# Kernel optimization log

Measured on AMD Instinct MI355X. Metric: run time of the kernel, lower is better.

Reference implementation:

```python
import jax, jax.numpy as jnp
import numpy as np

B, T, C = 4, 2048, 512
H, CDR_HEADS = 8, 2
D = C // H


def setup_inputs() -> dict:
    key = jax.random.key(0)
    ks = jax.random.split(key, 12)
    s = 1.0 / np.sqrt(C)
    return {
        "x": jax.random.normal(ks[0], (B, T, C), dtype=jnp.float32),
        "mask": jax.random.randint(ks[1], (B, T), 0, 2, dtype=jnp.int32),
        "cdrs_score": jax.random.randint(ks[2], (B, T), 0, 2, dtype=jnp.int32),
        "Wq": jax.random.normal(ks[3], (C, C), dtype=jnp.float32) * s,
        "bq": jnp.zeros((C,), dtype=jnp.float32),
        "Wk": jax.random.normal(ks[4], (C, C), dtype=jnp.float32) * s,
        "bk": jnp.zeros((C,), dtype=jnp.float32),
        "Wv": jax.random.normal(ks[5], (C, C), dtype=jnp.float32) * s,
        "bv": jnp.zeros((C,), dtype=jnp.float32),
        "Wo": jax.random.normal(ks[6], (C, C), dtype=jnp.float32) * s,
        "bo": jnp.zeros((C,), dtype=jnp.float32),
    }


def reference(x, mask, cdrs_score, Wq, bq, Wk, bk, Wv, bv, Wo, bo):
    # projections -> [B, H, T, D]
    def heads(y):
        return y.reshape(B, T, H, D).transpose(0, 2, 1, 3)

    q = heads(x @ Wq + bq)
    k = heads(x @ Wk + bk)
    v = heads(x @ Wv + bv)

    scores = jnp.einsum("bhqd,bhkd->bhqk", q, k) / jnp.sqrt(jnp.float32(D))

    # padding mask: keys with mask==0 are invalid for all heads
    pad = (mask == 0)[:, None, None, :]                      # [B,1,1,T]
    scores = jnp.where(pad, -jnp.inf, scores)

    # CDR key mask for the first CDR_HEADS heads; disabled if a sample has no CDR tokens
    cdr_key_mask = (cdrs_score == 0)                          # [B, T]
    all_masked = jnp.all(cdr_key_mask, axis=-1, keepdims=True)  # [B, 1]
    cdr_key_mask = jnp.where(all_masked, False, cdr_key_mask)   # [B, T]
    head_is_cdr = (jnp.arange(H) < CDR_HEADS)[None, :, None, None]  # [1,H,1,1]
    cdr_full = head_is_cdr & cdr_key_mask[:, None, None, :]         # [B,H,1,T]
    scores = jnp.where(cdr_full, -jnp.inf, scores)

    attn = jax.nn.softmax(scores, axis=-1)                    # [B,H,T,T]
    ctx = jnp.einsum("bhqk,bhkd->bhqd", attn, v)
    ctx = ctx.transpose(0, 2, 1, 3).reshape(B, T, C)
    return ctx @ Wo + bo
```

## Files before the change

### kernel.cpp

```cpp
#include <hip/hip_runtime.h>
#include <math.h>

#define B_ 4
#define T_ 2048
#define C_ 512
#define H_ 8
#define D_ 64
#define CDR_HEADS_ 2
#define NROWS (B_ * T_)

typedef unsigned short ush;
typedef __bf16  bf16x8 __attribute__((ext_vector_type(8)));
typedef float   f32x4  __attribute__((ext_vector_type(4)));

#define MFMA16(a, b, c) __builtin_amdgcn_mfma_f32_16x16x32_bf16((a), (b), (c), 0, 0, 0)

static __device__ __forceinline__ ush f2bf(float f) {
    unsigned u = __float_as_uint(f);
    u += 0x7FFF + ((u >> 16) & 1);
    return (ush)(u >> 16);
}
static __device__ __forceinline__ float bf2f(ush h) {
    return __uint_as_float(((unsigned)h) << 16);
}

static __device__ __forceinline__ void gload16(const void* gsrc, void* ldst) {
    __builtin_amdgcn_global_load_lds(
        (const __attribute__((address_space(1))) unsigned int*)gsrc,
        (__attribute__((address_space(3))) unsigned int*)ldst, 16, 0, 0);
}

__global__ __launch_bounds__(256) void compact_kernel(
    const int* __restrict__ mask, const int* __restrict__ cdrs,
    int* __restrict__ klist, int* __restrict__ kcnt) {
    __shared__ int s_any;
    __shared__ int sa[256], sb[256];
    const int b = blockIdx.x, tid = threadIdx.x;
    if (tid == 0) s_any = 0;
    __syncthreads();

    int m8[8], c8[8];
    int any = 0, ca = 0;
    const int base = b * T_ + tid * 8;
#pragma unroll
    for (int i = 0; i < 8; ++i) {
        m8[i] = mask[base + i];
        c8[i] = cdrs[base + i];
        any |= c8[i];
        ca += (m8[i] != 0);
    }
    if (any) s_any = 1;
    __syncthreads();
    const int en = s_any;

    int cb = 0;
#pragma unroll
    for (int i = 0; i < 8; ++i)
        cb += (m8[i] != 0 && (!en || c8[i] != 0));

    sa[tid] = ca; sb[tid] = cb;
    __syncthreads();
    for (int off = 1; off < 256; off <<= 1) {
        int va = 0, vb = 0;
        if (tid >= off) { va = sa[tid - off]; vb = sb[tid - off]; }
        __syncthreads();
        sa[tid] += va; sb[tid] += vb;
        __syncthreads();
    }

    int offA = sa[tid] - ca;
    int offB = sb[tid] - cb;
    int* la = klist + (size_t)(b * 2 + 0) * T_;
    int* lb = klist + (size_t)(b * 2 + 1) * T_;
#pragma unroll
    for (int i = 0; i < 8; ++i) {
        const int t = tid * 8 + i;
        if (m8[i] != 0) la[offA++] = t;
        if (m8[i] != 0 && (!en || c8[i] != 0)) lb[offB++] = t;
    }
    if (tid == 255) {
        kcnt[b * 2 + 0] = sa[255];
        kcnt[b * 2 + 1] = sb[255];
    }
}

__global__ __launch_bounds__(256) void decomp_a_kernel(
    const float* __restrict__ src, ush* __restrict__ Dh, ush* __restrict__ Dl) {
    const int id = blockIdx.x * 256 + threadIdx.x;
    const int m = id >> 6, kc = id & 63;
    const float* p = src + (size_t)m * C_ + kc * 8;
    const float4 a = ((const float4*)p)[0];
    const float4 b2 = ((const float4*)p)[1];
    float xv[8] = {a.x, a.y, a.z, a.w, b2.x, b2.y, b2.z, b2.w};
    union { ush u[8]; int4 q; } hi, lo;
#pragma unroll
    for (int i = 0; i < 8; ++i) {
        const ush h = f2bf(xv[i]);
        hi.u[i] = h;
        lo.u[i] = f2bf(xv[i] - bf2f(h));
    }
    const int mt = m >> 7, ml = m & 127, kt = kc >> 2, cidx = kc & 3;
    const size_t tbase = ((size_t)mt * 16 + kt) * 4096;
    const int boff = ml * 64 + ((cidx ^ ((ml >> 1) & 3)) << 4);
    *(int4*)((char*)(Dh + tbase) + boff) = hi.q;
    *(int4*)((char*)(Dl + tbase) + boff) = lo.q;
}

__global__ __launch_bounds__(256) void decomp_w_kernel(
    const float* __restrict__ W0, const float* __restrict__ W1,
    const float* __restrict__ W2, const float* __restrict__ W3,
    ush* __restrict__ Wth, ush* __restrict__ Wtl) {
    const int mat = blockIdx.y;
    const float* W = (mat == 0) ? W0 : (mat == 1) ? W1 : (mat == 2) ? W2 : W3;
    const int id = blockIdx.x * 256 + threadIdx.x;
    const int n = id & 511, kc = id >> 9;
    float xv[8];
#pragma unroll
    for (int j = 0; j < 8; ++j)
        xv[j] = W[(size_t)(kc * 8 + j) * C_ + n];
    union { ush u[8]; int4 q; } hi, lo;
#pragma unroll
    for (int i = 0; i < 8; ++i) {
        const ush h = f2bf(xv[i]);
        hi.u[i] = h;
        lo.u[i] = f2bf(xv[i] - bf2f(h));
    }
    const int nt = n >> 7, nl = n & 127, kt = kc >> 2, cidx = kc & 3;
    const size_t tbase = (size_t)mat * 262144 + ((size_t)nt * 16 + kt) * 4096;
    const int boff = nl * 64 + ((cidx ^ ((nl >> 1) & 3)) << 4);
    *(int4*)((char*)(Wth + tbase) + boff) = hi.q;
    *(int4*)((char*)(Wtl + tbase) + boff) = lo.q;
}

template <int OUTMODE>
static __device__ __forceinline__ void gemm3_body(
    const ush* __restrict__ Ah_g, const ush* __restrict__ Al_g,
    const ush* __restrict__ Bh_g, const ush* __restrict__ Bl_g,
    const float* __restrict__ bias, void* __restrict__ outp, float scale) {
    __shared__ char lds[32768];
    char* const sAh = lds;
    char* const sAl = lds + 8192;
    char* const sBh = lds + 16384;
    char* const sBl = lds + 24576;

    const int tid = threadIdx.x;
    const int lane = tid & 63, w = tid >> 6;
    const int g = lane >> 4, l15 = lane & 15;
    const int wr = w >> 1, wc = w & 1;
    const int mt = blockIdx.x, nt = blockIdx.y;

    const char* gAh = (const char*)Ah_g + (size_t)(mt * 16) * 8192;
    const char* gAl = (const char*)Al_g + (size_t)(mt * 16) * 8192;
    const char* gBh = (const char*)Bh_g + (size_t)(nt * 16) * 8192;
    const char* gBl = (const char*)Bl_g + (size_t)(nt * 16) * 8192;

    f32x4 acc[4][4];
#pragma unroll
    for (int i = 0; i < 4; ++i)
#pragma unroll
        for (int j = 0; j < 4; ++j)
#pragma unroll
            for (int r = 0; r < 4; ++r) acc[i][j][r] = 0.f;

    const int lw = w * 2048;
    for (int kt = 0; kt < 16; ++kt) {
        __syncthreads();
        const size_t gb = (size_t)kt * 8192 + lw + lane * 16;
        gload16(gAh + gb,        sAh + lw);
        gload16(gAh + gb + 1024, sAh + lw + 1024);
        gload16(gAl + gb,        sAl + lw);
        gload16(gAl + gb + 1024, sAl + lw + 1024);
        gload16(gBh + gb,        sBh + lw);
        gload16(gBh + gb + 1024, sBh + lw + 1024);
        gload16(gBl + gb,        sBl + lw);
        gload16(gBl + gb + 1024, sBl + lw + 1024);
        __syncthreads();

        bf16x8 fah[4], fal[4], fbh[4], fbl[4];
#pragma unroll
        for (int rb = 0; rb < 4; ++rb) {
            const int row = wr * 64 + rb * 16 + l15;
            const int off = row * 64 + ((g ^ ((row >> 1) & 3)) << 4);
            fah[rb] = __builtin_bit_cast(bf16x8, *(const int4*)(sAh + off));
            fal[rb] = __builtin_bit_cast(bf16x8, *(const int4*)(sAl + off));
        }
#pragma unroll
        for (int cb = 0; cb < 4; ++cb) {
            const int row = wc * 64 + cb * 16 + l15;
            const int off = row * 64 + ((g ^ ((row >> 1) & 3)) << 4);
            fbh[cb] = __builtin_bit_cast(bf16x8, *(const int4*)(sBh + off));
            fbl[cb] = __builtin_bit_cast(bf16x8, *(const int4*)(sBl + off));
        }
#pragma unroll
        for (int rb = 0; rb < 4; ++rb)
#pragma unroll
            for (int cb = 0; cb < 4; ++cb) {
                acc[rb][cb] = MFMA16(fah[rb], fbh[cb], acc[rb][cb]);
                acc[rb][cb] = MFMA16(fah[rb], fbl[cb], acc[rb][cb]);
                acc[rb][cb] = MFMA16(fal[rb], fbh[cb], acc[rb][cb]);
            }
    }

    const int mbase = mt * 128 + wr * 64;
    const int nbase = nt * 128 + wc * 64;
    float bcol[4];
#pragma unroll
    for (int cb = 0; cb < 4; ++cb) bcol[cb] = bias[nbase + cb * 16 + l15];

#pragma unroll
    for (int rb = 0; rb < 4; ++rb)
#pragma unroll
        for (int cb = 0; cb < 4; ++cb) {
            const int colg = nbase + cb * 16 + l15;
#pragma unroll
            for (int r = 0; r < 4; ++r) {
                const int m = mbase + rb * 16 + g * 4 + r;
                const float vv = acc[rb][cb][r] + bcol[cb];
                if (OUTMODE == 0) {
                    ((float*)outp)[(size_t)m * C_ + colg] = vv;
                } else {
                    const int bb = m >> 11, t = m & (T_ - 1);
                    const int h = colg >> 6, d = colg & 63;
                    ((ush*)outp)[(((size_t)(bb * H_ + h) * T_ + t) * D_) + d] =
                        f2bf(vv * scale);
                }
            }
        }
}

__global__ __launch_bounds__(256) void gemm3_qkv_kernel(
    const ush* __restrict__ Xh, const ush* __restrict__ Xl,
    const ush* __restrict__ Wth, const ush* __restrict__ Wtl,
    const float* __restrict__ bq, const float* __restrict__ bk,
    const float* __restrict__ bv,
    ush* __restrict__ Qb, ush* __restrict__ Kb, ush* __restrict__ Vb) {
    const int z = blockIdx.z;
    const ush* bh = Wth + (size_t)z * 262144;
    const ush* bl = Wtl + (size_t)z * 262144;
    if (z == 0)      gemm3_body<1>(Xh, Xl, bh, bl, bq, Qb, 0.125f);
    else if (z == 1) gemm3_body<1>(Xh, Xl, bh, bl, bk, Kb, 1.0f);
    else             gemm3_body<1>(Xh, Xl, bh, bl, bv, Vb, 1.0f);
}

__global__ __launch_bounds__(256) void gemm3_out_kernel(
    const ush* __restrict__ Ch, const ush* __restrict__ Cl,
    const ush* __restrict__ Wth, const ush* __restrict__ Wtl,
    const float* __restrict__ bo, float* __restrict__ out) {
    gemm3_body<0>(Ch, Cl, Wth + (size_t)3 * 262144, Wtl + (size_t)3 * 262144,
                  bo, out, 1.0f);
}

__global__ __launch_bounds__(256) void gather_kernel(
    const ush* __restrict__ Kb, const ush* __restrict__ Vb,
    const int* __restrict__ klist, const int* __restrict__ kcnt,
    ush* __restrict__ Kc, ush* __restrict__ Vct) {
    __shared__ ush Vs[64 * 72];
    const int tid = threadIdx.x;
    const int ti = blockIdx.x, h = blockIdx.y, b = blockIdx.z;
    const int sel = (h < CDR_HEADS_) ? 1 : 0;
    const int NV = kcnt[b * 2 + sel];
    if (ti * 64 >= NV) return;
    const int* __restrict__ list = klist + (size_t)(b * 2 + sel) * T_;
    const size_t bh = (size_t)b * H_ + h;
    const ush* kb_ = Kb + bh * T_ * D_;
    const ush* vb_ = Vb + bh * T_ * D_;
    ush* kt = Kc + bh * (32 * 4096) + (size_t)ti * 4096;
    ush* vt = Vct + bh * (32 * 4096) + (size_t)ti * 4096;

    const int i = tid >> 2, c = tid & 3;
    const int pos = ti * 64 + i;
    int4 kv0 = {0,0,0,0}, kv1 = {0,0,0,0}, vv0 = {0,0,0,0}, vv1 = {0,0,0,0};
    if (pos < NV) {
        const int row = list[pos];
        const int4* kr = (const int4*)(kb_ + (size_t)row * D_ + c * 16);
        kv0 = kr[0]; kv1 = kr[1];
        const int4* vr = (const int4*)(vb_ + (size_t)row * D_ + c * 16);
        vv0 = vr[0]; vv1 = vr[1];
    }
    {
        const int s0 = (c * 2) ^ (i & 7), s1 = (c * 2 + 1) ^ (i & 7);
        *(int4*)(kt + i * 64 + s0 * 8) = kv0;
        *(int4*)(kt + i * 64 + s1 * 8) = kv1;
    }
    *(int4*)(Vs + i * 72 + c * 16)     = vv0;
    *(int4*)(Vs + i * 72 + c * 16 + 8) = vv1;
    __syncthreads();
    {
        const int d = tid >> 2, c2 = tid & 3;
        union { ush u[16]; int4 q[2]; } pk;
#pragma unroll
        for (int ii = 0; ii < 16; ++ii)
            pk.u[ii] = Vs[(c2 * 16 + ii) * 72 + d];
        const int s0 = (c2 * 2) ^ (d & 7), s1 = (c2 * 2 + 1) ^ (d & 7);
        *(int4*)(vt + d * 64 + s0 * 8) = pk.q[0];
        *(int4*)(vt + d * 64 + s1 * 8) = pk.q[1];
    }
}

__global__ __launch_bounds__(256) void attn_mfma_kernel(
    const ush* __restrict__ Qb, const ush* __restrict__ Kc,
    const ush* __restrict__ Vct, const int* __restrict__ kcnt,
    float* __restrict__ ctx) {
    __shared__ ush Ks[2][4096];
    __shared__ ush Vts[2][4096];
    __shared__ ush Pl[4 * 32 * 72];

    const int tid = threadIdx.x;
    const int lane = tid & 63, w = tid >> 6;
    const int g = lane >> 4, l15 = lane & 15;
    const int qt = blockIdx.x, h = blockIdx.y, b = blockIdx.z;
    const int sel = (h < CDR_HEADS_) ? 1 : 0;
    const int NV = kcnt[b * 2 + sel];
    const int ntiles = (NV + 63) >> 6;
    const size_t bh = (size_t)b * H_ + h;
    const int swz = (l15 & 7) << 4;

    bf16x8 aq[2][2];
    {
        const ush* qp = Qb + (bh * T_ + (size_t)qt * 128 + w * 32) * D_;
#pragma unroll
        for (int qb = 0; qb < 2; ++qb)
#pragma unroll
            for (int kc = 0; kc < 2; ++kc) {
                int4 t4 = *(const int4*)(qp + (qb * 16 + l15) * D_ + kc * 32 + g * 8);
                aq[qb][kc] = __builtin_bit_cast(bf16x8, t4);
            }
    }

    f32x4 cacc[2][4];
#pragma unroll
    for (int qb = 0; qb < 2; ++qb)
#pragma unroll
        for (int db = 0; db < 4; ++db)
#pragma unroll
            for (int r = 0; r < 4; ++r) cacc[qb][db][r] = 0.f;
    float mr[2] = {-INFINITY, -INFINITY};
    float lr[2] = {0.f, 0.f};

    const char* ktiles = (const char*)(Kc + bh * (32 * 4096));
    const char* vtiles = (const char*)(Vct + bh * (32 * 4096));
    ush* Pw = Pl + w * (32 * 72);
    const int lw = w * 1024;

    gload16(ktiles + lw * 2 + lane * 16, &Ks[0][lw]);
    gload16(ktiles + lw * 2 + 1024 + lane * 16, &Ks[0][lw + 512]);
    gload16(vtiles + lw * 2 + lane * 16, &Vts[0][lw]);
    gload16(vtiles + lw * 2 + 1024 + lane * 16, &Vts[0][lw + 512]);
    __syncthreads();

    for (int t = 0; t < ntiles; ++t) {
        const int cur = t & 1, nxt = cur ^ 1;
        if (t + 1 < ntiles) {
            const char* gk = ktiles + (size_t)(t + 1) * 8192 + lw * 2 + lane * 16;
            const char* gv = vtiles + (size_t)(t + 1) * 8192 + lw * 2 + lane * 16;
            gload16(gk, &Ks[nxt][lw]);
            gload16(gk + 1024, &Ks[nxt][lw + 512]);
            gload16(gv, &Vts[nxt][lw]);
            gload16(gv + 1024, &Vts[nxt][lw + 512]);
        }

        bf16x8 bk[4][2];
#pragma unroll
        for (int j = 0; j < 4; ++j) {
            const int rowb = (j * 16 + l15) * 128;
            bk[j][0] = __builtin_bit_cast(bf16x8,
                *(const int4*)((const char*)Ks[cur] + ((rowb + g * 16) ^ swz)));
            bk[j][1] = __builtin_bit_cast(bf16x8,
                *(const int4*)((const char*)Ks[cur] + ((rowb + 64 + g * 16) ^ swz)));
        }
        f32x4 s[2][4];
        const f32x4 z4 = {0.f, 0.f, 0.f, 0.f};
        __builtin_amdgcn_s_setprio(1);
#pragma unroll
        for (int j = 0; j < 4; ++j) s[0][j] = MFMA16(bk[j][0], aq[0][0], z4);
#pragma unroll
        for (int j = 0; j < 4; ++j) s[1][j] = MFMA16(bk[j][0], aq[1][0], z4);
#pragma unroll
        for (int j = 0; j < 4; ++j) s[0][j] = MFMA16(bk[j][1], aq[0][1], s[0][j]);
#pragma unroll
        for (int j = 0; j < 4; ++j) s[1][j] = MFMA16(bk[j][1], aq[1][1], s[1][j]);
        __builtin_amdgcn_s_setprio(0);

        const int kb0 = t * 64;
        if (kb0 + 64 > NV) {
#pragma unroll
            for (int j = 0; j < 4; ++j)
#pragma unroll
                for (int r = 0; r < 4; ++r)
                    if (kb0 + j * 16 + g * 4 + r >= NV) {
                        s[0][j][r] = -INFINITY;
                        s[1][j][r] = -INFINITY;
                    }
        }

        float rq[2];
#pragma unroll
        for (int qb = 0; qb < 2; ++qb) {
            float mx = s[qb][0][0];
#pragma unroll
            for (int j = 0; j < 4; ++j)
#pragma unroll
                for (int r = 0; r < 4; ++r) mx = fmaxf(mx, s[qb][j][r]);
            mx = fmaxf(mx, __shfl_xor(mx, 16));
            mx = fmaxf(mx, __shfl_xor(mx, 32));
            const float mn = fmaxf(mr[qb], mx);
            rq[qb] = __expf(mr[qb] - mn);
            mr[qb] = mn;
            float sum = 0.f;
#pragma unroll
            for (int j = 0; j < 4; ++j)
#pragma unroll
                for (int r = 0; r < 4; ++r) {
                    const float p = __expf(s[qb][j][r] - mn);
                    s[qb][j][r] = p;
                    sum += p;
                }
            sum += __shfl_xor(sum, 16);
            sum += __shfl_xor(sum, 32);
            lr[qb] = lr[qb] * rq[qb] + sum;
        }

#pragma unroll
        for (int qb = 0; qb < 2; ++qb)
#pragma unroll
            for (int r = 0; r < 4; ++r) {
                const float rr = __shfl(rq[qb], g * 4 + r, 16);
#pragma unroll
                for (int db = 0; db < 4; ++db) cacc[qb][db][r] *= rr;
            }

#pragma unroll
        for (int qb = 0; qb < 2; ++qb) {
            unsigned* prow = (unsigned*)(Pw + (qb * 16 + l15) * 72);
#pragma unroll
            for (int j = 0; j < 4; ++j) {
                const unsigned p01 = (unsigned)f2bf(s[qb][j][0]) |
                                     ((unsigned)f2bf(s[qb][j][1]) << 16);
                const unsigned p23 = (unsigned)f2bf(s[qb][j][2]) |
                                     ((unsigned)f2bf(s[qb][j][3]) << 16);
                prow[(j * 16 + g * 4) >> 1] = p01;
                prow[(j * 16 + g * 4 + 2) >> 1] = p23;
            }
        }

        __builtin_amdgcn_s_setprio(1);
#pragma unroll
        for (int kc = 0; kc < 2; ++kc) {
            bf16x8 pa0 = __builtin_bit_cast(bf16x8,
                *(const int4*)(Pw + l15 * 72 + kc * 32 + g * 8));
            bf16x8 pa1 = __builtin_bit_cast(bf16x8,
                *(const int4*)(Pw + (16 + l15) * 72 + kc * 32 + g * 8));
#pragma unroll
            for (int db = 0; db < 4; ++db) {
                bf16x8 vbf = __builtin_bit_cast(bf16x8,
                    *(const int4*)((const char*)Vts[cur] +
                        ((((db * 16 + l15) * 128) + kc * 64 + g * 16) ^ swz)));
                cacc[0][db] = MFMA16(pa0, vbf, cacc[0][db]);
                cacc[1][db] = MFMA16(pa1, vbf, cacc[1][db]);
            }
        }
        __builtin_amdgcn_s_setprio(0);

        __syncthreads();
    }

    const size_t trow = (size_t)b * T_ + (size_t)qt * 128 + w * 32;
#pragma unroll
    for (int qb = 0; qb < 2; ++qb)
#pragma unroll
        for (int r = 0; r < 4; ++r) {
            const float lrq = __shfl(lr[qb], g * 4 + r, 16);
            const float inv = 1.f / lrq;
            float* orow = ctx + (trow + qb * 16 + g * 4 + r) * C_ + h * D_;
#pragma unroll
            for (int db = 0; db < 4; ++db)
                orow[db * 16 + l15] = cacc[qb][db][r] * inv;
        }
}

extern "C" void kernel_launch(void* const* d_in, const int* in_sizes, int n_in,
                              void* d_out, int out_size, void* d_ws, size_t ws_size,
                              hipStream_t stream) {
    const float* x    = (const float*)d_in[0];
    const int*   mask = (const int*)d_in[1];
    const int*   cdrs = (const int*)d_in[2];
    const float* Wq   = (const float*)d_in[3];
    const float* bq   = (const float*)d_in[4];
    const float* Wk   = (const float*)d_in[5];
    const float* bk   = (const float*)d_in[6];
    const float* Wv   = (const float*)d_in[7];
    const float* bv   = (const float*)d_in[8];
    const float* Wo   = (const float*)d_in[9];
    const float* bo   = (const float*)d_in[10];
    float* out = (float*)d_out;

    const size_t per = (size_t)B_ * H_ * T_ * D_;
    ush* Qb  = (ush*)d_ws;
    ush* Kb  = Qb + per;
    ush* Vb  = Kb + per;
    ush* Kc  = Vb + per;
    ush* Vct = Kc + per;
    ush* Xh  = Vct + per;
    ush* Xl  = Xh + per;
    ush* Wth = Xl + per;
    ush* Wtl = Wth + 4 * 262144;
    int* klist = (int*)(Wtl + 4 * 262144);
    int* kcnt  = klist + (size_t)B_ * 2 * T_;
    float* ctxf = (float*)Kb;

    compact_kernel<<<B_, 256, 0, stream>>>(mask, cdrs, klist, kcnt);

    decomp_a_kernel<<<2048, 256, 0, stream>>>(x, Xh, Xl);
    decomp_w_kernel<<<dim3(128, 4), 256, 0, stream>>>(Wq, Wk, Wv, Wo, Wth, Wtl);

    gemm3_qkv_kernel<<<dim3(64, 4, 3), 256, 0, stream>>>(
        Xh, Xl, Wth, Wtl, bq, bk, bv, Qb, Kb, Vb);

    gather_kernel<<<dim3(32, H_, B_), 256, 0, stream>>>(Kb, Vb, klist, kcnt,
                                                        Kc, Vct);

    attn_mfma_kernel<<<dim3(T_ / 128, H_, B_), 256, 0, stream>>>(
        Qb, Kc, Vct, kcnt, ctxf);

    decomp_a_kernel<<<2048, 256, 0, stream>>>(ctxf, Xh, Xl);

    gemm3_out_kernel<<<dim3(64, 4), 256, 0, stream>>>(Xh, Xl, Wth, Wtl, bo, out);
}
```

Measured before the change: 222.9 us.

## Merge prep kernels and fuse ctx bf16 split into attention epilogue

Merges the mask compaction and the x and W bf16 hi/lo decomposition kernels into one prep launch. The attention kernel now writes ctx directly as swizzled bf16 hi/lo tiles, which removes the fp32 ctx round trip and the second decomposition kernel. Attention is also restructured to 512 threads with 16 query rows per wave. It remaps blocks in a flat 1D grid, adds a lazy rescale that skips the online-softmax correction when the running max rises by at most 8, and uses an XOR-swizzled P buffer. The cost is scattered 2-byte global stores in the epilogue and more waves per block sharing the same LDS K/V tiles.

```diff
diff --git a/kernel.cpp b/kernel.cpp
--- a/kernel.cpp
+++ b/kernel.cpp
@@ -30,106 +30,104 @@
         (__attribute__((address_space(3))) unsigned int*)ldst, 16, 0, 0);
 }
 
-__global__ __launch_bounds__(256) void compact_kernel(
+__global__ __launch_bounds__(256) void prep_kernel(
+    const float* __restrict__ x,
+    const float* __restrict__ W0, const float* __restrict__ W1,
+    const float* __restrict__ W2, const float* __restrict__ W3,
     const int* __restrict__ mask, const int* __restrict__ cdrs,
+    ush* __restrict__ Xh, ush* __restrict__ Xl,
+    ush* __restrict__ Wth, ush* __restrict__ Wtl,
     int* __restrict__ klist, int* __restrict__ kcnt) {
     __shared__ int s_any;
     __shared__ int sa[256], sb[256];
-    const int b = blockIdx.x, tid = threadIdx.x;
-    if (tid == 0) s_any = 0;
-    __syncthreads();
-
-    int m8[8], c8[8];
-    int any = 0, ca = 0;
-    const int base = b * T_ + tid * 8;
-#pragma unroll
-    for (int i = 0; i < 8; ++i) {
-        m8[i] = mask[base + i];
-        c8[i] = cdrs[base + i];
-        any |= c8[i];
-        ca += (m8[i] != 0);
-    }
-    if (any) s_any = 1;
-    __syncthreads();
-    const int en = s_any;
-
-    int cb = 0;
-#pragma unroll
-    for (int i = 0; i < 8; ++i)
-        cb += (m8[i] != 0 && (!en || c8[i] != 0));
-
-    sa[tid] = ca; sb[tid] = cb;
-    __syncthreads();
-    for (int off = 1; off < 256; off <<= 1) {
-        int va = 0, vb = 0;
-        if (tid >= off) { va = sa[tid - off]; vb = sb[tid - off]; }
+    const int bid = blockIdx.x, tid = threadIdx.x;
+
+    if (bid < 2048) {
+        const int id = bid * 256 + tid;
+        const int m = id >> 6, kc = id & 63;
+        const float* p = x + (size_t)m * C_ + kc * 8;
+        const float4 a = ((const float4*)p)[0];
+        const float4 b2 = ((const float4*)p)[1];
+        float xv[8] = {a.x, a.y, a.z, a.w, b2.x, b2.y, b2.z, b2.w};
+        union { ush u[8]; int4 q; } hi, lo;
+#pragma unroll
+        for (int i = 0; i < 8; ++i) {
+            const ush h = f2bf(xv[i]);
+            hi.u[i] = h;
+            lo.u[i] = f2bf(xv[i] - bf2f(h));
+        }
+        const int mt = m >> 7, ml = m & 127, kt = kc >> 2, cidx = kc & 3;
+        const size_t tbase = ((size_t)mt * 16 + kt) * 4096;
+        const int boff = ml * 64 + ((cidx ^ ((ml >> 1) & 3)) << 4);
+        *(int4*)((char*)(Xh + tbase) + boff) = hi.q;
+        *(int4*)((char*)(Xl + tbase) + boff) = lo.q;
+    } else if (bid < 2560) {
+        const int z = bid - 2048;
+        const int mat = z >> 7;
+        const float* W = (mat == 0) ? W0 : (mat == 1) ? W1 : (mat == 2) ? W2 : W3;
+        const int id = (z & 127) * 256 + tid;
+        const int n = id & 511, kc = id >> 9;
+        float xv[8];
+#pragma unroll
+        for (int j = 0; j < 8; ++j)
+            xv[j] = W[(size_t)(kc * 8 + j) * C_ + n];
+        union { ush u[8]; int4 q; } hi, lo;
+#pragma unroll
+        for (int i = 0; i < 8; ++i) {
+            const ush h = f2bf(xv[i]);
+            hi.u[i] = h;
+            lo.u[i] = f2bf(xv[i] - bf2f(h));
+        }
+        const int nt = n >> 7, nl = n & 127, kt = kc >> 2, cidx = kc & 3;
+        const size_t tbase = (size_t)mat * 262144 + ((size_t)nt * 16 + kt) * 4096;
+        const int boff = nl * 64 + ((cidx ^ ((nl >> 1) & 3)) << 4);
+        *(int4*)((char*)(Wth + tbase) + boff) = hi.q;
+        *(int4*)((char*)(Wtl + tbase) + boff) = lo.q;
+    } else {
+        const int b = bid - 2560;
+        if (tid == 0) s_any = 0;
         __syncthreads();
-        sa[tid] += va; sb[tid] += vb;
+        int m8[8], c8[8];
+        int any = 0, ca = 0;
+        const int base = b * T_ + tid * 8;
+#pragma unroll
+        for (int i = 0; i < 8; ++i) {
+            m8[i] = mask[base + i];
+            c8[i] = cdrs[base + i];
+            any |= c8[i];
+            ca += (m8[i] != 0);
+        }
+        if (any) s_any = 1;
         __syncthreads();
-    }
-
-    int offA = sa[tid] - ca;
-    int offB = sb[tid] - cb;
-    int* la = klist + (size_t)(b * 2 + 0) * T_;
-    int* lb = klist + (size_t)(b * 2 + 1) * T_;
-#pragma unroll
-    for (int i = 0; i < 8; ++i) {
-        const int t = tid * 8 + i;
-        if (m8[i] != 0) la[offA++] = t;
-        if (m8[i] != 0 && (!en || c8[i] != 0)) lb[offB++] = t;
-    }
-    if (tid == 255) {
-        kcnt[b * 2 + 0] = sa[255];
-        kcnt[b * 2 + 1] = sb[255];
-    }
-}
-
-__global__ __launch_bounds__(256) void decomp_a_kernel(
-    const float* __restrict__ src, ush* __restrict__ Dh, ush* __restrict__ Dl) {
-    const int id = blockIdx.x * 256 + threadIdx.x;
-    const int m = id >> 6, kc = id & 63;
-    const float* p = src + (size_t)m * C_ + kc * 8;
-    const float4 a = ((const float4*)p)[0];
-    const float4 b2 = ((const float4*)p)[1];
-    float xv[8] = {a.x, a.y, a.z, a.w, b2.x, b2.y, b2.z, b2.w};
-    union { ush u[8]; int4 q; } hi, lo;
-#pragma unroll
-    for (int i = 0; i < 8; ++i) {
-        const ush h = f2bf(xv[i]);
-        hi.u[i] = h;
-        lo.u[i] = f2bf(xv[i] - bf2f(h));
-    }
-    const int mt = m >> 7, ml = m & 127, kt = kc >> 2, cidx = kc & 3;
-    const size_t tbase = ((size_t)mt * 16 + kt) * 4096;
-    const int boff = ml * 64 + ((cidx ^ ((ml >> 1) & 3)) << 4);
-    *(int4*)((char*)(Dh + tbase) + boff) = hi.q;
-    *(int4*)((char*)(Dl + tbase) + boff) = lo.q;
-}
-
-__global__ __launch_bounds__(256) void decomp_w_kernel(
-    const float* __restrict__ W0, const float* __restrict__ W1,
-    const float* __restrict__ W2, const float* __restrict__ W3,
-    ush* __restrict__ Wth, ush* __restrict__ Wtl) {
-    const int mat = blockIdx.y;
-    const float* W = (mat == 0) ? W0 : (mat == 1) ? W1 : (mat == 2) ? W2 : W3;
-    const int id = blockIdx.x * 256 + threadIdx.x;
-    const int n = id & 511, kc = id >> 9;
-    float xv[8];
-#pragma unroll
-    for (int j = 0; j < 8; ++j)
-        xv[j] = W[(size_t)(kc * 8 + j) * C_ + n];
-    union { ush u[8]; int4 q; } hi, lo;
-#pragma unroll
-    for (int i = 0; i < 8; ++i) {
-        const ush h = f2bf(xv[i]);
-        hi.u[i] = h;
-        lo.u[i] = f2bf(xv[i] - bf2f(h));
-    }
-    const int nt = n >> 7, nl = n & 127, kt = kc >> 2, cidx = kc & 3;
-    const size_t tbase = (size_t)mat * 262144 + ((size_t)nt * 16 + kt) * 4096;
-    const int boff = nl * 64 + ((cidx ^ ((nl >> 1) & 3)) << 4);
-    *(int4*)((char*)(Wth + tbase) + boff) = hi.q;
-    *(int4*)((char*)(Wtl + tbase) + boff) = lo.q;
+        const int en = s_any;
+        int cb = 0;
+#pragma unroll
+        for (int i = 0; i < 8; ++i)
+            cb += (m8[i] != 0 && (!en || c8[i] != 0));
+        sa[tid] = ca; sb[tid] = cb;
+        __syncthreads();
+        for (int off = 1; off < 256; off <<= 1) {
+            int va = 0, vb = 0;
+            if (tid >= off) { va = sa[tid - off]; vb = sb[tid - off]; }
+            __syncthreads();
+            sa[tid] += va; sb[tid] += vb;
+            __syncthreads();
+        }
+        int offA = sa[tid] - ca;
+        int offB = sb[tid] - cb;
+        int* la = klist + (size_t)(b * 2 + 0) * T_;
+        int* lb = klist + (size_t)(b * 2 + 1) * T_;
+#pragma unroll
+        for (int i = 0; i < 8; ++i) {
+            const int t = tid * 8 + i;
+            if (m8[i] != 0) la[offA++] = t;
+            if (m8[i] != 0 && (!en || c8[i] != 0)) lb[offB++] = t;
+        }
+        if (tid == 255) {
+            kcnt[b * 2 + 0] = sa[255];
+            kcnt[b * 2 + 1] = sb[255];
+        }
+    }
 }
 
 template <int OUTMODE>
@@ -297,66 +295,62 @@
     }
 }
 
-__global__ __launch_bounds__(256) void attn_mfma_kernel(
+__global__ __launch_bounds__(512) void attn_mfma_kernel(
     const ush* __restrict__ Qb, const ush* __restrict__ Kc,
     const ush* __restrict__ Vct, const int* __restrict__ kcnt,
-    float* __restrict__ ctx) {
+    ush* __restrict__ Xh, ush* __restrict__ Xl) {
     __shared__ ush Ks[2][4096];
     __shared__ ush Vts[2][4096];
-    __shared__ ush Pl[4 * 32 * 72];
+    __shared__ ush Pl[8192];
 
     const int tid = threadIdx.x;
     const int lane = tid & 63, w = tid >> 6;
     const int g = lane >> 4, l15 = lane & 15;
-    const int qt = blockIdx.x, h = blockIdx.y, b = blockIdx.z;
+
+    const int i = blockIdx.x;
+    const int x7 = i & 7, local = i >> 3;
+    const int b = local >> 4;
+    const int h = (x7 - 2 * b) & 7;
+    const int qt = local & 15;
+    const int bh = b * H_ + h;
+
     const int sel = (h < CDR_HEADS_) ? 1 : 0;
     const int NV = kcnt[b * 2 + sel];
     const int ntiles = (NV + 63) >> 6;
-    const size_t bh = (size_t)b * H_ + h;
     const int swz = (l15 & 7) << 4;
 
-    bf16x8 aq[2][2];
+    bf16x8 aq[2];
     {
-        const ush* qp = Qb + (bh * T_ + (size_t)qt * 128 + w * 32) * D_;
-#pragma unroll
-        for (int qb = 0; qb < 2; ++qb)
-#pragma unroll
-            for (int kc = 0; kc < 2; ++kc) {
-                int4 t4 = *(const int4*)(qp + (qb * 16 + l15) * D_ + kc * 32 + g * 8);
-                aq[qb][kc] = __builtin_bit_cast(bf16x8, t4);
-            }
-    }
-
-    f32x4 cacc[2][4];
-#pragma unroll
-    for (int qb = 0; qb < 2; ++qb)
-#pragma unroll
-        for (int db = 0; db < 4; ++db)
-#pragma unroll
-            for (int r = 0; r < 4; ++r) cacc[qb][db][r] = 0.f;
-    float mr[2] = {-INFINITY, -INFINITY};
-    float lr[2] = {0.f, 0.f};
-
-    const char* ktiles = (const char*)(Kc + bh * (32 * 4096));
-    const char* vtiles = (const char*)(Vct + bh * (32 * 4096));
-    ush* Pw = Pl + w * (32 * 72);
-    const int lw = w * 1024;
-
-    gload16(ktiles + lw * 2 + lane * 16, &Ks[0][lw]);
-    gload16(ktiles + lw * 2 + 1024 + lane * 16, &Ks[0][lw + 512]);
-    gload16(vtiles + lw * 2 + lane * 16, &Vts[0][lw]);
-    gload16(vtiles + lw * 2 + 1024 + lane * 16, &Vts[0][lw + 512]);
+        const ush* qp = Qb + ((size_t)bh * T_ + qt * 128 + w * 16) * D_;
+#pragma unroll
+        for (int kc = 0; kc < 2; ++kc)
+            aq[kc] = __builtin_bit_cast(bf16x8,
+                *(const int4*)(qp + l15 * D_ + kc * 32 + g * 8));
+    }
+
+    f32x4 cacc[4];
+#pragma unroll
+    for (int db = 0; db < 4; ++db)
+#pragma unroll
+        for (int r = 0; r < 4; ++r) cacc[db][r] = 0.f;
+    float mr = -INFINITY, lr = 0.f;
+
+    const char* ktiles = (const char*)(Kc + (size_t)bh * (32 * 4096));
+    const char* vtiles = (const char*)(Vct + (size_t)bh * (32 * 4096));
+    char* Pw = (char*)Pl + w * 2048;
+    const int lwo = w * 512;
+
+    gload16(ktiles + lwo * 2 + lane * 16, &Ks[0][lwo]);
+    gload16(vtiles + lwo * 2 + lane * 16, &Vts[0][lwo]);
     __syncthreads();
 
     for (int t = 0; t < ntiles; ++t) {
         const int cur = t & 1, nxt = cur ^ 1;
         if (t + 1 < ntiles) {
-            const char* gk = ktiles + (size_t)(t + 1) * 8192 + lw * 2 + lane * 16;
-            const char* gv = vtiles + (size_t)(t + 1) * 8192 + lw * 2 + lane * 16;
-            gload16(gk, &Ks[nxt][lw]);
-            gload16(gk + 1024, &Ks[nxt][lw + 512]);
-            gload16(gv, &Vts[nxt][lw]);
-            gload16(gv + 1024, &Vts[nxt][lw + 512]);
+            gload16(ktiles + (size_t)(t + 1) * 8192 + lwo * 2 + lane * 16,
+                    &Ks[nxt][lwo]);
+            gload16(vtiles + (size_t)(t + 1) * 8192 + lwo * 2 + lane * 16,
+                    &Vts[nxt][lwo]);
         }
 
         bf16x8 bk[4][2];
@@ -368,17 +362,13 @@
             bk[j][1] = __builtin_bit_cast(bf16x8,
                 *(const int4*)((const char*)Ks[cur] + ((rowb + 64 + g * 16) ^ swz)));
         }
-        f32x4 s[2][4];
+        f32x4 s[4];
         const f32x4 z4 = {0.f, 0.f, 0.f, 0.f};
         __builtin_amdgcn_s_setprio(1);
 #pragma unroll
-        for (int j = 0; j < 4; ++j) s[0][j] = MFMA16(bk[j][0], aq[0][0], z4);
-#pragma unroll
-        for (int j = 0; j < 4; ++j) s[1][j] = MFMA16(bk[j][0], aq[1][0], z4);
-#pragma unroll
-        for (int j = 0; j < 4; ++j) s[0][j] = MFMA16(bk[j][1], aq[0][1], s[0][j]);
-#pragma unroll
-        for (int j = 0; j < 4; ++j) s[1][j] = MFMA16(bk[j][1], aq[1][1], s[1][j]);
+        for (int j = 0; j < 4; ++j) s[j] = MFMA16(bk[j][0], aq[0], z4);
+#pragma unroll
+        for (int j = 0; j < 4; ++j) s[j] = MFMA16(bk[j][1], aq[1], s[j]);
         __builtin_amdgcn_s_setprio(0);
 
         const int kb0 = t * 64;
@@ -387,95 +377,94 @@
             for (int j = 0; j < 4; ++j)
 #pragma unroll
                 for (int r = 0; r < 4; ++r)
-                    if (kb0 + j * 16 + g * 4 + r >= NV) {
-                        s[0][j][r] = -INFINITY;
-                        s[1][j][r] = -INFINITY;
-                    }
-        }
-
-        float rq[2];
-#pragma unroll
-        for (int qb = 0; qb < 2; ++qb) {
-            float mx = s[qb][0][0];
-#pragma unroll
-            for (int j = 0; j < 4; ++j)
-#pragma unroll
-                for (int r = 0; r < 4; ++r) mx = fmaxf(mx, s[qb][j][r]);
-            mx = fmaxf(mx, __shfl_xor(mx, 16));
-            mx = fmaxf(mx, __shfl_xor(mx, 32));
-            const float mn = fmaxf(mr[qb], mx);
-            rq[qb] = __expf(mr[qb] - mn);
-            mr[qb] = mn;
-            float sum = 0.f;
-#pragma unroll
-            for (int j = 0; j < 4; ++j)
-#pragma unroll
-                for (int r = 0; r < 4; ++r) {
-                    const float p = __expf(s[qb][j][r] - mn);
-                    s[qb][j][r] = p;
-                    sum += p;
-                }
-            sum += __shfl_xor(sum, 16);
-            sum += __shfl_xor(sum, 32);
-            lr[qb] = lr[qb] * rq[qb] + sum;
-        }
-
-#pragma unroll
-        for (int qb = 0; qb < 2; ++qb)
+                    if (kb0 + j * 16 + g * 4 + r >= NV) s[j][r] = -INFINITY;
+        }
+
+        float pmax = s[0][0];
+#pragma unroll
+        for (int j = 0; j < 4; ++j)
+#pragma unroll
+            for (int r = 0; r < 4; ++r) pmax = fmaxf(pmax, s[j][r]);
+        pmax = fmaxf(pmax, __shfl_xor(pmax, 16));
+        pmax = fmaxf(pmax, __shfl_xor(pmax, 32));
+        if (!__all(pmax <= mr + 8.f)) {
+            const float mn = fmaxf(mr, pmax);
+            const float rr = __expf(mr - mn);
+            mr = mn;
+            lr *= rr;
 #pragma unroll
             for (int r = 0; r < 4; ++r) {
-                const float rr = __shfl(rq[qb], g * 4 + r, 16);
-#pragma unroll
-                for (int db = 0; db < 4; ++db) cacc[qb][db][r] *= rr;
+                const float rrq = __shfl(rr, g * 4 + r, 16);
+#pragma unroll
+                for (int db = 0; db < 4; ++db) cacc[db][r] *= rrq;
             }
-
-#pragma unroll
-        for (int qb = 0; qb < 2; ++qb) {
-            unsigned* prow = (unsigned*)(Pw + (qb * 16 + l15) * 72);
-#pragma unroll
-            for (int j = 0; j < 4; ++j) {
-                const unsigned p01 = (unsigned)f2bf(s[qb][j][0]) |
-                                     ((unsigned)f2bf(s[qb][j][1]) << 16);
-                const unsigned p23 = (unsigned)f2bf(s[qb][j][2]) |
-                                     ((unsigned)f2bf(s[qb][j][3]) << 16);
-                prow[(j * 16 + g * 4) >> 1] = p01;
-                prow[(j * 16 + g * 4 + 2) >> 1] = p23;
+        }
+        float sum = 0.f;
+#pragma unroll
+        for (int j = 0; j < 4; ++j)
+#pragma unroll
+            for (int r = 0; r < 4; ++r) {
+                const float p = __expf(s[j][r] - mr);
+                s[j][r] = p;
+                sum += p;
             }
-        }
-
+        sum += __shfl_xor(sum, 16);
+        sum += __shfl_xor(sum, 32);
+        lr += sum;
+
+#pragma unroll
+        for (int j = 0; j < 4; ++j) {
+            const ush u0 = __builtin_bit_cast(ush, (__bf16)s[j][0]);
+            const ush u1 = __builtin_bit_cast(ush, (__bf16)s[j][1]);
+            const ush u2 = __builtin_bit_cast(ush, (__bf16)s[j][2]);
+            const ush u3 = __builtin_bit_cast(ush, (__bf16)s[j][3]);
+            uint2 pk;
+            pk.x = (unsigned)u0 | ((unsigned)u1 << 16);
+            pk.y = (unsigned)u2 | ((unsigned)u3 << 16);
+            const int sb = (j * 2 + (g >> 1)) ^ (l15 & 7);
+            *(uint2*)(Pw + l15 * 128 + sb * 16 + (g & 1) * 8) = pk;
+        }
+
+        bf16x8 pa[2];
+#pragma unroll
+        for (int kc = 0; kc < 2; ++kc)
+            pa[kc] = __builtin_bit_cast(bf16x8,
+                *(const int4*)(Pw + l15 * 128 + (((kc * 4 + g) ^ (l15 & 7)) << 4)));
         __builtin_amdgcn_s_setprio(1);
 #pragma unroll
-        for (int kc = 0; kc < 2; ++kc) {
-            bf16x8 pa0 = __builtin_bit_cast(bf16x8,
-                *(const int4*)(Pw + l15 * 72 + kc * 32 + g * 8));
-            bf16x8 pa1 = __builtin_bit_cast(bf16x8,
-                *(const int4*)(Pw + (16 + l15) * 72 + kc * 32 + g * 8));
+        for (int kc = 0; kc < 2; ++kc)
 #pragma unroll
             for (int db = 0; db < 4; ++db) {
                 bf16x8 vbf = __builtin_bit_cast(bf16x8,
                     *(const int4*)((const char*)Vts[cur] +
                         ((((db * 16 + l15) * 128) + kc * 64 + g * 16) ^ swz)));
-                cacc[0][db] = MFMA16(pa0, vbf, cacc[0][db]);
-                cacc[1][db] = MFMA16(pa1, vbf, cacc[1][db]);
+                cacc[db] = MFMA16(pa[kc], vbf, cacc[db]);
             }
-        }
         __builtin_amdgcn_s_setprio(0);
 
         __syncthreads();
     }
 
-    const size_t trow = (size_t)b * T_ + (size_t)qt * 128 + w * 32;
-#pragma unroll
-    for (int qb = 0; qb < 2; ++qb)
-#pragma unroll
-        for (int r = 0; r < 4; ++r) {
-            const float lrq = __shfl(lr[qb], g * 4 + r, 16);
-            const float inv = 1.f / lrq;
-            float* orow = ctx + (trow + qb * 16 + g * 4 + r) * C_ + h * D_;
-#pragma unroll
-            for (int db = 0; db < 4; ++db)
-                orow[db * 16 + l15] = cacc[qb][db][r] * inv;
-        }
+    const int mt = b * 16 + qt;
+#pragma unroll
+    for (int r = 0; r < 4; ++r) {
+        const float lrq = __shfl(lr, g * 4 + r, 16);
+        const float inv = 1.f / lrq;
+        const int ml = w * 16 + g * 4 + r;
+#pragma unroll
+        for (int db = 0; db < 4; ++db) {
+            const int col = h * 64 + db * 16 + l15;
+            const float val = cacc[db][r] * inv;
+            const __bf16 hb = (__bf16)val;
+            const __bf16 lb2 = (__bf16)(val - (float)hb);
+            const int kt2 = col >> 5;
+            const int cidx = (col >> 3) & 3;
+            const size_t tb = ((size_t)mt * 16 + kt2) * 4096;
+            const int boff = ml * 64 + ((cidx ^ ((ml >> 1) & 3)) << 4) + (l15 & 7) * 2;
+            *(ush*)((char*)(Xh + tb) + boff) = __builtin_bit_cast(ush, hb);
+            *(ush*)((char*)(Xl + tb) + boff) = __builtin_bit_cast(ush, lb2);
+        }
+    }
 }
 
 extern "C" void kernel_launch(void* const* d_in, const int* in_sizes, int n_in,
@@ -506,12 +495,9 @@
     ush* Wtl = Wth + 4 * 262144;
     int* klist = (int*)(Wtl + 4 * 262144);
     int* kcnt  = klist + (size_t)B_ * 2 * T_;
-    float* ctxf = (float*)Kb;
-
-    compact_kernel<<<B_, 256, 0, stream>>>(mask, cdrs, klist, kcnt);
-
-    decomp_a_kernel<<<2048, 256, 0, stream>>>(x, Xh, Xl);
-    decomp_w_kernel<<<dim3(128, 4), 256, 0, stream>>>(Wq, Wk, Wv, Wo, Wth, Wtl);
+
+    prep_kernel<<<2564, 256, 0, stream>>>(x, Wq, Wk, Wv, Wo, mask, cdrs,
+                                          Xh, Xl, Wth, Wtl, klist, kcnt);
 
     gemm3_qkv_kernel<<<dim3(64, 4, 3), 256, 0, stream>>>(
         Xh, Xl, Wth, Wtl, bq, bk, bv, Qb, Kb, Vb);
@@ -519,10 +505,7 @@
     gather_kernel<<<dim3(32, H_, B_), 256, 0, stream>>>(Kb, Vb, klist, kcnt,
                                                         Kc, Vct);
 
-    attn_mfma_kernel<<<dim3(T_ / 128, H_, B_), 256, 0, stream>>>(
-        Qb, Kc, Vct, kcnt, ctxf);
-
-    decomp_a_kernel<<<2048, 256, 0, stream>>>(ctxf, Xh, Xl);
+    attn_mfma_kernel<<<512, 512, 0, stream>>>(Qb, Kc, Vct, kcnt, Xh, Xl);
 
     gemm3_out_kernel<<<dim3(64, 4), 256, 0, stream>>>(Xh, Xl, Wth, Wtl, bo, out);
 }
```

After: 198.5 us. -10.9%, faster.
